# Performance work log

Hardware: AMD Instinct MI355X
Metric: run time of the kernel (lower is better)

## Reference

```python
import jax, jax.numpy as jnp
import numpy as np

DT = 0.1
B, L, IN_SZ, MEM = 64, 2048, 128, 256


def setup_inputs() -> dict:
    key = jax.random.key(0)
    ks = jax.random.split(key, 13)
    u = jax.random.normal(ks[0], (B, L, IN_SZ), dtype=jnp.float32)
    s_in = 1.0 / np.sqrt(IN_SZ)
    s_h = 1.0 / np.sqrt(MEM)
    def w_in(k):
        return jax.random.normal(k, (MEM, IN_SZ), dtype=jnp.float32) * s_in
    def w_h(k):
        return jax.random.normal(k, (MEM, MEM), dtype=jnp.float32) * s_h
    return {
        "u": u,
        "Wia": w_in(ks[1]), "Wha": w_h(ks[2]),
        "Wib": w_in(ks[3]), "Whb": w_h(ks[4]),
        "Wic": w_in(ks[5]), "Whc": w_h(ks[6]),
        "Wid": w_in(ks[7]), "Whd": w_h(ks[8]),
        "Wie": w_in(ks[9]), "Whe": w_h(ks[10]),
        "Wio": w_in(ks[11]),
    }


def _run(u, Wia, Wha, Wib, Whb, Wic, Whc, Wid, Whd, Wie, Whe, Wio):
    # Precompute all 6 input projections once: [L, B, MEM] each (time-major for scan)
    Win = jnp.stack([Wia, Wib, Wic, Wid, Wie, Wio], axis=0)  # [6, MEM, IN]
    xproj = jnp.einsum("blk,gmk->lgbm", u, Win)  # [L, 6, B, MEM]

    hf0 = jnp.zeros((u.shape[0], Wha.shape[0]), dtype=u.dtype)
    hs0 = jnp.zeros_like(hf0)

    def step(carry, xs):
        hf, hs = carry
        xa, xb, xc, xd, xe, xo = xs[0], xs[1], xs[2], xs[3], xs[4], xs[5]
        a = 1.0 + jnp.tanh(xa + hf @ Wha.T)
        b = 1.5 * (1.0 + jnp.tanh(xb + hf @ Whb.T))
        c = 3.0 * DT + (1.0 - 3.0 * DT) * jax.nn.sigmoid(xc + hf @ Whc.T)
        d = 0.3 * DT * jax.nn.sigmoid(xd + hf @ Whd.T)
        e = 1.0 + jax.nn.sigmoid(xe + hf @ Whe.T)
        hfn = (1.0 - c) * hf + c * jnp.tanh(xo + (a + b * hf * hf - hs) * hf)
        hsn = hs * (1.0 - d) + d * (e * hf) ** 4
        return (hfn, hsn), hfn

    _, hseq = jax.lax.scan(step, (hf0, hs0), xproj)  # [L, B, MEM]
    hseq = jnp.transpose(hseq, (1, 0, 2))  # [B, L, MEM]
    return hseq


def reference(u, Wia, Wha, Wib, Whb, Wic, Whc, Wid, Whd, Wie, Whe, Wio):
    hseq = _run(u, Wia, Wha, Wib, Whb, Wic, Whc, Wid, Whd, Wie, Whe, Wio)
    return hseq, hseq[:, -1:, :]
```

## Files before the change

kernel.cpp:

```cpp
#include <hip/hip_runtime.h>
#include <hip/hip_fp16.h>

#define L_SEQ 2048
#define N_B   64
#define IN_K  128
#define MEM_N 256

typedef float    f32x4 __attribute__((ext_vector_type(4)));
typedef _Float16 f16x8 __attribute__((ext_vector_type(8)));

__device__ __forceinline__ float rcp_f(float x) { return __builtin_amdgcn_rcpf(x); }
__device__ __forceinline__ float tanh_f(float x) {
    return 1.0f - 2.0f * rcp_f(__expf(2.0f * x) + 1.0f);
}
__device__ __forceinline__ float sig_f(float x) {
    return rcp_f(1.0f + __expf(-x));
}

__device__ __forceinline__ void split8(const float* v, f16x8& hi, f16x8& lo) {
#pragma unroll
    for (int i = 0; i < 8; ++i) {
        _Float16 h = (_Float16)v[i];
        hi[i] = h;
        lo[i] = (_Float16)(v[i] - (float)h);
    }
}

__global__ void __launch_bounds__(256, 1)
befrc_scan(const float* __restrict__ u,
           const float* __restrict__ Wia, const float* __restrict__ Wha,
           const float* __restrict__ Wib, const float* __restrict__ Whb,
           const float* __restrict__ Wic, const float* __restrict__ Whc,
           const float* __restrict__ Wid, const float* __restrict__ Whd,
           const float* __restrict__ Wie, const float* __restrict__ Whe,
           const float* __restrict__ Wio,
           float* __restrict__ out,
           unsigned long long* __restrict__ pubq)
{
    const int wg  = blockIdx.x;
    const int g   = wg & 3;
    const int s   = wg >> 2;
    const int tid = threadIdx.x;
    const int w   = tid >> 6;
    const int l   = tid & 63;
    const int lq  = l >> 4;
    const int lr  = l & 15;

    __shared__ __align__(16) float red[2][6][4][16][16];

    const float* Wi[6] = {Wia, Wib, Wic, Wid, Wie, Wio};
    const float* Wh[5] = {Wha, Whb, Whc, Whd, Whe};

    const int mrow = s * 16 + lr;
    f16x8 whf_hi[5][2], whf_lo[5][2];
#pragma unroll
    for (int gg = 0; gg < 5; ++gg) {
#pragma unroll
        for (int cc = 0; cc < 2; ++cc) {
            const int k0 = (2 * w + cc) * 32 + lq * 4;
            const float* p = Wh[gg] + mrow * MEM_N + k0;
            float4 f0 = *(const float4*)p;
            float4 f1 = *(const float4*)(p + 16);
            float v[8] = {f0.x, f0.y, f0.z, f0.w, f1.x, f1.y, f1.z, f1.w};
            split8(v, whf_hi[gg][cc], whf_lo[gg][cc]);
        }
    }
    f16x8 wif_hi[6], wif_lo[6];
#pragma unroll
    for (int gg = 0; gg < 6; ++gg) {
        const int k0 = w * 32 + lq * 4;
        const float* p = Wi[gg] + mrow * IN_K + k0;
        float4 f0 = *(const float4*)p;
        float4 f1 = *(const float4*)(p + 16);
        float v[8] = {f0.x, f0.y, f0.z, f0.w, f1.x, f1.y, f1.z, f1.w};
        split8(v, wif_hi[gg], wif_lo[gg]);
    }

    const int eb    = tid >> 4;
    const int em    = tid & 15;
    const int bglob = g * 16 + eb;
    const int mglob = s * 16 + em;
    float hf_loc = 0.0f, hs_loc = 0.0f;

    const int  bfrag  = g * 16 + lr;
    const long u_base = (long)bfrag * L_SEQ * IN_K + w * 32 + lq * 4;
    const int  k0a    = (2 * w + 0) * 32 + lq * 4;
    const int  k0b    = (2 * w + 1) * 32 + lq * 4;

    float4 uf0 = *(const float4*)(u + u_base);
    float4 uf1 = *(const float4*)(u + u_base + 16);

    float* const out_row = out + (long)bglob * L_SEQ * MEM_N + mglob;

    for (int t = 0; t < L_SEQ; ++t) {
        f32x4 acc[6];
#pragma unroll
        for (int gg = 0; gg < 6; ++gg) acc[gg] = (f32x4){0.f, 0.f, 0.f, 0.f};
        {
            float v[8] = {uf0.x, uf0.y, uf0.z, uf0.w, uf1.x, uf1.y, uf1.z, uf1.w};
            f16x8 ub_hi, ub_lo;
            split8(v, ub_hi, ub_lo);
#pragma unroll
            for (int gg = 0; gg < 6; ++gg) {
                acc[gg] = __builtin_amdgcn_mfma_f32_16x16x32_f16(wif_hi[gg], ub_hi, acc[gg], 0, 0, 0);
                acc[gg] = __builtin_amdgcn_mfma_f32_16x16x32_f16(wif_hi[gg], ub_lo, acc[gg], 0, 0, 0);
                acc[gg] = __builtin_amdgcn_mfma_f32_16x16x32_f16(wif_lo[gg], ub_hi, acc[gg], 0, 0, 0);
            }
        }

        unsigned long long q[16];
        {
            const unsigned tgt = (unsigned)t;
            const unsigned long long* pb =
                pubq + (size_t)(t & 1) * N_B * MEM_N + (size_t)bfrag * MEM_N;
            int spins = 0;
            for (;;) {
#pragma unroll
                for (int i = 0; i < 4; ++i) {
                    q[i]      = __hip_atomic_load(pb + k0a + i,      __ATOMIC_RELAXED, __HIP_MEMORY_SCOPE_AGENT);
                    q[4 + i]  = __hip_atomic_load(pb + k0a + 16 + i, __ATOMIC_RELAXED, __HIP_MEMORY_SCOPE_AGENT);
                    q[8 + i]  = __hip_atomic_load(pb + k0b + i,      __ATOMIC_RELAXED, __HIP_MEMORY_SCOPE_AGENT);
                    q[12 + i] = __hip_atomic_load(pb + k0b + 16 + i, __ATOMIC_RELAXED, __HIP_MEMORY_SCOPE_AGENT);
                }
                int ok = 1;
#pragma unroll
                for (int i = 0; i < 16; ++i)
                    ok &= ((unsigned)(q[i] >> 32) == tgt);
                if (__all(ok) || ++spins > (1 << 18)) break;
                __builtin_amdgcn_s_sleep(1);
            }
        }

#pragma unroll
        for (int cc = 0; cc < 2; ++cc) {
            f16x8 hb_hi, hb_lo;
#pragma unroll
            for (int j = 0; j < 8; ++j) {
                const unsigned pay = (unsigned)q[cc * 8 + j];
                hb_hi[j] = __builtin_bit_cast(_Float16, (unsigned short)(pay & 0xffff));
                hb_lo[j] = __builtin_bit_cast(_Float16, (unsigned short)(pay >> 16));
            }
#pragma unroll
            for (int gg = 0; gg < 5; ++gg) {
                acc[gg] = __builtin_amdgcn_mfma_f32_16x16x32_f16(whf_hi[gg][cc], hb_hi, acc[gg], 0, 0, 0);
                acc[gg] = __builtin_amdgcn_mfma_f32_16x16x32_f16(whf_hi[gg][cc], hb_lo, acc[gg], 0, 0, 0);
                acc[gg] = __builtin_amdgcn_mfma_f32_16x16x32_f16(whf_lo[gg][cc], hb_hi, acc[gg], 0, 0, 0);
            }
        }

        const int pb2 = t & 1;
#pragma unroll
        for (int gg = 0; gg < 6; ++gg)
            *(f32x4*)&red[pb2][gg][w][lr][lq * 4] = acc[gg];
        __syncthreads();

        float pre[6];
#pragma unroll
        for (int gg = 0; gg < 6; ++gg)
            pre[gg] = red[pb2][gg][0][eb][em] + red[pb2][gg][1][eb][em]
                    + red[pb2][gg][2][eb][em] + red[pb2][gg][3][eb][em];

        {
            const long ub = u_base + (long)((t + 1 < L_SEQ) ? t + 1 : t) * IN_K;
            uf0 = *(const float4*)(u + ub);
            uf1 = *(const float4*)(u + ub + 16);
        }

        const float hf_old = hf_loc, hs_old = hs_loc;
        {
            const float av  = 1.0f + tanh_f(pre[0]);
            const float bv  = 1.5f * (1.0f + tanh_f(pre[1]));
            const float cv  = 0.3f  + 0.7f * sig_f(pre[2]);
            const float arg = pre[5] + (av + bv * hf_old * hf_old - hs_old) * hf_old;
            hf_loc = (1.0f - cv) * hf_old + cv * tanh_f(arg);
        }
        {
            const _Float16 ph = (_Float16)hf_loc;
            const _Float16 pl = (_Float16)(hf_loc - (float)ph);
            const unsigned pay = (unsigned)__builtin_bit_cast(unsigned short, ph)
                               | ((unsigned)__builtin_bit_cast(unsigned short, pl) << 16);
            const unsigned long long val = ((unsigned long long)(unsigned)(t + 1) << 32) | pay;
            const size_t po = (size_t)((t + 1) & 1) * N_B * MEM_N
                            + (size_t)bglob * MEM_N + mglob;
            __hip_atomic_store(pubq + po, val, __ATOMIC_RELAXED, __HIP_MEMORY_SCOPE_AGENT);
        }

        {
            const float dv  = 0.03f * sig_f(pre[3]);
            const float ev  = 1.0f + sig_f(pre[4]);
            const float eh  = ev * hf_old;
            const float eh2 = eh * eh;
            hs_loc = hs_old * (1.0f - dv) + dv * (eh2 * eh2);
        }
        out_row[(long)t * MEM_N] = hf_loc;
    }

    out[(long)N_B * L_SEQ * MEM_N + (long)bglob * MEM_N + mglob] = hf_loc;
}

extern "C" void kernel_launch(void* const* d_in, const int* in_sizes, int n_in,
                              void* d_out, int out_size, void* d_ws, size_t ws_size,
                              hipStream_t stream) {
    (void)in_sizes; (void)n_in; (void)out_size; (void)ws_size;
    const float* u   = (const float*)d_in[0];
    const float* Wia = (const float*)d_in[1];
    const float* Wha = (const float*)d_in[2];
    const float* Wib = (const float*)d_in[3];
    const float* Whb = (const float*)d_in[4];
    const float* Wic = (const float*)d_in[5];
    const float* Whc = (const float*)d_in[6];
    const float* Wid = (const float*)d_in[7];
    const float* Whd = (const float*)d_in[8];
    const float* Wie = (const float*)d_in[9];
    const float* Whe = (const float*)d_in[10];
    const float* Wio = (const float*)d_in[11];

    float* out = (float*)d_out;
    unsigned long long* pubq = (unsigned long long*)d_ws;

    hipMemsetAsync(d_ws, 0, (size_t)2 * N_B * MEM_N * sizeof(unsigned long long), stream);

    befrc_scan<<<dim3(64), dim3(256), 0, stream>>>(
        u, Wia, Wha, Wib, Whb, Wic, Whc, Wid, Whd, Wie, Whe, Wio,
        out, pubq);
}
```

Baseline: 6.899 ms.

## Reorder recurrent step: poll peers first, then input projection, with inline-asm loads

The spin-wait now polls the published hidden state first, using eight wide inline-asm global loads with cache-bypass bits instead of sixteen 64-bit atomic loads, and drops the s_sleep. The input-projection MFMAs and the prefetch of the next u slice move after the wait, so they no longer sit in front of it. The LDS reduction buffer is padded to reduce bank conflicts, the barrier is a raw s_barrier, and the d/e gate reductions are deferred until after the hf publish to shorten the critical path. The costs are inline-asm fragility around waitcnt handling and the loss of independent input work that could previously hide the wait latency.

Result: faster. 5.616 ms (-18.6%).

```diff
diff --git a/kernel.cpp b/kernel.cpp
--- a/kernel.cpp
+++ b/kernel.cpp
@@ -8,6 +8,7 @@
 
 typedef float    f32x4 __attribute__((ext_vector_type(4)));
 typedef _Float16 f16x8 __attribute__((ext_vector_type(8)));
+typedef unsigned u32x4 __attribute__((ext_vector_type(4)));
 
 __device__ __forceinline__ float rcp_f(float x) { return __builtin_amdgcn_rcpf(x); }
 __device__ __forceinline__ float tanh_f(float x) {
@@ -46,7 +47,7 @@
     const int lq  = l >> 4;
     const int lr  = l & 15;
 
-    __shared__ __align__(16) float red[2][6][4][16][16];
+    __shared__ __align__(16) float red[2][6][4][16][20];
 
     const float* Wi[6] = {Wia, Wib, Wic, Wid, Wie, Wio};
     const float* Wh[5] = {Wha, Whb, Whc, Whd, Whe};
@@ -87,58 +88,92 @@
     const int  k0a    = (2 * w + 0) * 32 + lq * 4;
     const int  k0b    = (2 * w + 1) * 32 + lq * 4;
 
-    float4 uf0 = *(const float4*)(u + u_base);
-    float4 uf1 = *(const float4*)(u + u_base + 16);
+    u32x4 ua, ub2;
+    {
+        const float* up = u + u_base;
+        asm volatile(
+            "global_load_dwordx4 %0, %2, off\n\t"
+            "global_load_dwordx4 %1, %3, off"
+            : "=v"(ua), "=v"(ub2)
+            : "v"(up), "v"(up + 16)
+            : "memory");
+    }
 
     float* const out_row = out + (long)bglob * L_SEQ * MEM_N + mglob;
 
+#pragma clang loop unroll(disable)
     for (int t = 0; t < L_SEQ; ++t) {
-        f32x4 acc[6];
-#pragma unroll
-        for (int gg = 0; gg < 6; ++gg) acc[gg] = (f32x4){0.f, 0.f, 0.f, 0.f};
-        {
-            float v[8] = {uf0.x, uf0.y, uf0.z, uf0.w, uf1.x, uf1.y, uf1.z, uf1.w};
-            f16x8 ub_hi, ub_lo;
-            split8(v, ub_hi, ub_lo);
-#pragma unroll
-            for (int gg = 0; gg < 6; ++gg) {
-                acc[gg] = __builtin_amdgcn_mfma_f32_16x16x32_f16(wif_hi[gg], ub_hi, acc[gg], 0, 0, 0);
-                acc[gg] = __builtin_amdgcn_mfma_f32_16x16x32_f16(wif_hi[gg], ub_lo, acc[gg], 0, 0, 0);
-                acc[gg] = __builtin_amdgcn_mfma_f32_16x16x32_f16(wif_lo[gg], ub_hi, acc[gg], 0, 0, 0);
-            }
-        }
-
-        unsigned long long q[16];
+        u32x4 r0, r1, r2, r3, r4, r5, r6, r7;
         {
             const unsigned tgt = (unsigned)t;
             const unsigned long long* pb =
                 pubq + (size_t)(t & 1) * N_B * MEM_N + (size_t)bfrag * MEM_N;
+            const unsigned long long* p0 = pb + k0a;
+            const unsigned long long* p1 = pb + k0a + 16;
+            const unsigned long long* p2 = pb + k0b;
+            const unsigned long long* p3 = pb + k0b + 16;
             int spins = 0;
             for (;;) {
-#pragma unroll
-                for (int i = 0; i < 4; ++i) {
-                    q[i]      = __hip_atomic_load(pb + k0a + i,      __ATOMIC_RELAXED, __HIP_MEMORY_SCOPE_AGENT);
-                    q[4 + i]  = __hip_atomic_load(pb + k0a + 16 + i, __ATOMIC_RELAXED, __HIP_MEMORY_SCOPE_AGENT);
-                    q[8 + i]  = __hip_atomic_load(pb + k0b + i,      __ATOMIC_RELAXED, __HIP_MEMORY_SCOPE_AGENT);
-                    q[12 + i] = __hip_atomic_load(pb + k0b + 16 + i, __ATOMIC_RELAXED, __HIP_MEMORY_SCOPE_AGENT);
-                }
-                int ok = 1;
-#pragma unroll
-                for (int i = 0; i < 16; ++i)
-                    ok &= ((unsigned)(q[i] >> 32) == tgt);
-                if (__all(ok) || ++spins > (1 << 18)) break;
-                __builtin_amdgcn_s_sleep(1);
-            }
-        }
-
+                asm volatile(
+                    "global_load_dwordx4 %0, %8, off sc0 sc1\n\t"
+                    "global_load_dwordx4 %1, %8, off offset:16 sc0 sc1\n\t"
+                    "global_load_dwordx4 %2, %9, off sc0 sc1\n\t"
+                    "global_load_dwordx4 %3, %9, off offset:16 sc0 sc1\n\t"
+                    "global_load_dwordx4 %4, %10, off sc0 sc1\n\t"
+                    "global_load_dwordx4 %5, %10, off offset:16 sc0 sc1\n\t"
+                    "global_load_dwordx4 %6, %11, off sc0 sc1\n\t"
+                    "global_load_dwordx4 %7, %11, off offset:16 sc0 sc1\n\t"
+                    "s_waitcnt vmcnt(0)"
+                    : "=v"(r0), "=v"(r1), "=v"(r2), "=v"(r3),
+                      "=v"(r4), "=v"(r5), "=v"(r6), "=v"(r7)
+                    : "v"(p0), "v"(p1), "v"(p2), "v"(p3)
+                    : "memory");
+                int ok = (r0[1] == tgt) & (r0[3] == tgt) & (r1[1] == tgt) & (r1[3] == tgt)
+                       & (r2[1] == tgt) & (r2[3] == tgt) & (r3[1] == tgt) & (r3[3] == tgt)
+                       & (r4[1] == tgt) & (r4[3] == tgt) & (r5[1] == tgt) & (r5[3] == tgt)
+                       & (r6[1] == tgt) & (r6[3] == tgt) & (r7[1] == tgt) & (r7[3] == tgt);
+                if (__all(ok) || ++spins > (1 << 17)) break;
+            }
+        }
+        __builtin_amdgcn_sched_barrier(0);
+
+        f32x4 acc[6];
+#pragma unroll
+        for (int gg = 0; gg < 6; ++gg) acc[gg] = (f32x4){0.f, 0.f, 0.f, 0.f};
+        {
+            float4 f0 = __builtin_bit_cast(float4, ua);
+            float4 f1 = __builtin_bit_cast(float4, ub2);
+            float v[8] = {f0.x, f0.y, f0.z, f0.w, f1.x, f1.y, f1.z, f1.w};
+            f16x8 uh, ul;
+            split8(v, uh, ul);
+#pragma unroll
+            for (int gg = 0; gg < 6; ++gg) {
+                acc[gg] = __builtin_amdgcn_mfma_f32_16x16x32_f16(wif_hi[gg], uh, acc[gg], 0, 0, 0);
+                acc[gg] = __builtin_amdgcn_mfma_f32_16x16x32_f16(wif_hi[gg], ul, acc[gg], 0, 0, 0);
+                acc[gg] = __builtin_amdgcn_mfma_f32_16x16x32_f16(wif_lo[gg], uh, acc[gg], 0, 0, 0);
+            }
+        }
+
+        {
+            const float* up = u + u_base + (long)((t + 1 < L_SEQ) ? t + 1 : t) * IN_K;
+            asm volatile(
+                "global_load_dwordx4 %0, %2, off\n\t"
+                "global_load_dwordx4 %1, %3, off"
+                : "=v"(ua), "=v"(ub2)
+                : "v"(up), "v"(up + 16)
+                : "memory");
+        }
+
+        unsigned pay[16] = {r0[0], r0[2], r1[0], r1[2], r2[0], r2[2], r3[0], r3[2],
+                            r4[0], r4[2], r5[0], r5[2], r6[0], r6[2], r7[0], r7[2]};
 #pragma unroll
         for (int cc = 0; cc < 2; ++cc) {
             f16x8 hb_hi, hb_lo;
 #pragma unroll
             for (int j = 0; j < 8; ++j) {
-                const unsigned pay = (unsigned)q[cc * 8 + j];
-                hb_hi[j] = __builtin_bit_cast(_Float16, (unsigned short)(pay & 0xffff));
-                hb_lo[j] = __builtin_bit_cast(_Float16, (unsigned short)(pay >> 16));
+                const unsigned p = pay[cc * 8 + j];
+                hb_hi[j] = __builtin_bit_cast(_Float16, (unsigned short)(p & 0xffff));
+                hb_lo[j] = __builtin_bit_cast(_Float16, (unsigned short)(p >> 16));
             }
 #pragma unroll
             for (int gg = 0; gg < 5; ++gg) {
@@ -152,42 +187,45 @@
 #pragma unroll
         for (int gg = 0; gg < 6; ++gg)
             *(f32x4*)&red[pb2][gg][w][lr][lq * 4] = acc[gg];
-        __syncthreads();
-
-        float pre[6];
-#pragma unroll
-        for (int gg = 0; gg < 6; ++gg)
-            pre[gg] = red[pb2][gg][0][eb][em] + red[pb2][gg][1][eb][em]
-                    + red[pb2][gg][2][eb][em] + red[pb2][gg][3][eb][em];
-
-        {
-            const long ub = u_base + (long)((t + 1 < L_SEQ) ? t + 1 : t) * IN_K;
-            uf0 = *(const float4*)(u + ub);
-            uf1 = *(const float4*)(u + ub + 16);
-        }
+        asm volatile("s_waitcnt lgkmcnt(0)\n\ts_barrier" ::: "memory");
+        __builtin_amdgcn_sched_barrier(0);
+
+        float pre0, pre1, pre2, pre5;
+        pre0 = red[pb2][0][0][eb][em] + red[pb2][0][1][eb][em]
+             + red[pb2][0][2][eb][em] + red[pb2][0][3][eb][em];
+        pre1 = red[pb2][1][0][eb][em] + red[pb2][1][1][eb][em]
+             + red[pb2][1][2][eb][em] + red[pb2][1][3][eb][em];
+        pre2 = red[pb2][2][0][eb][em] + red[pb2][2][1][eb][em]
+             + red[pb2][2][2][eb][em] + red[pb2][2][3][eb][em];
+        pre5 = red[pb2][5][0][eb][em] + red[pb2][5][1][eb][em]
+             + red[pb2][5][2][eb][em] + red[pb2][5][3][eb][em];
 
         const float hf_old = hf_loc, hs_old = hs_loc;
         {
-            const float av  = 1.0f + tanh_f(pre[0]);
-            const float bv  = 1.5f * (1.0f + tanh_f(pre[1]));
-            const float cv  = 0.3f  + 0.7f * sig_f(pre[2]);
-            const float arg = pre[5] + (av + bv * hf_old * hf_old - hs_old) * hf_old;
+            const float av  = 1.0f + tanh_f(pre0);
+            const float bv  = 1.5f * (1.0f + tanh_f(pre1));
+            const float cv  = 0.3f  + 0.7f * sig_f(pre2);
+            const float arg = pre5 + (av + bv * hf_old * hf_old - hs_old) * hf_old;
             hf_loc = (1.0f - cv) * hf_old + cv * tanh_f(arg);
         }
         {
             const _Float16 ph = (_Float16)hf_loc;
             const _Float16 pl = (_Float16)(hf_loc - (float)ph);
-            const unsigned pay = (unsigned)__builtin_bit_cast(unsigned short, ph)
+            const unsigned paw = (unsigned)__builtin_bit_cast(unsigned short, ph)
                                | ((unsigned)__builtin_bit_cast(unsigned short, pl) << 16);
-            const unsigned long long val = ((unsigned long long)(unsigned)(t + 1) << 32) | pay;
+            const unsigned long long val = ((unsigned long long)(unsigned)(t + 1) << 32) | paw;
             const size_t po = (size_t)((t + 1) & 1) * N_B * MEM_N
                             + (size_t)bglob * MEM_N + mglob;
             __hip_atomic_store(pubq + po, val, __ATOMIC_RELAXED, __HIP_MEMORY_SCOPE_AGENT);
         }
 
         {
-            const float dv  = 0.03f * sig_f(pre[3]);
-            const float ev  = 1.0f + sig_f(pre[4]);
+            const float pre3 = red[pb2][3][0][eb][em] + red[pb2][3][1][eb][em]
+                             + red[pb2][3][2][eb][em] + red[pb2][3][3][eb][em];
+            const float pre4 = red[pb2][4][0][eb][em] + red[pb2][4][1][eb][em]
+                             + red[pb2][4][2][eb][em] + red[pb2][4][3][eb][em];
+            const float dv  = 0.03f * sig_f(pre3);
+            const float ev  = 1.0f + sig_f(pre4);
             const float eh  = ev * hf_old;
             const float eh2 = eh * eh;
             hs_loc = hs_old * (1.0f - dv) + dv * (eh2 * eh2);
```
